# Kernel optimization log

Measured on AMD Instinct MI355X. Metric: run time of the kernel, lower is better.

The kernel has to match this reference:

```python
import jax, jax.numpy as jnp
import numpy as np

B, H, W, C = 8, 128, 128, 64


def setup_inputs() -> dict:
    key = jax.random.key(0)
    x = jax.random.normal(key, (B, H, W, C), dtype=jnp.float32)
    return {"x": x}


def reference(x):
    # Criss-cross affinity: for each pixel (i,j), dot products against
    # the rest of its row (order: k<j then k>j) followed by its full column.
    b, h, w, c = x.shape
    # Row affinities: [B,H,W,W], A_row[b,i,j,k] = <x[b,i,j], x[b,i,k]>
    a_row = jnp.einsum('bijc,bikc->bijk', x, x)
    # Column affinities: [B,H,W,H], A_col[b,i,j,m] = <x[b,i,j], x[b,m,j]>
    a_col = jnp.einsum('bijc,bmjc->bijm', x, x)
    # Remove the self entry k=j from row affinities, preserving order
    # [0..j-1, j+1..W-1] to match the original tf.concat.
    idx = np.array([[k for k in range(w) if k != j] for j in range(w)],
                   dtype=np.int32)  # [W, W-1]
    row_part = jnp.take_along_axis(a_row, jnp.asarray(idx)[None, None, :, :],
                                   axis=3)  # [B,H,W,W-1]
    # Output: [B, H, W, (W-1)+H]
    return jnp.concatenate([row_part, a_col], axis=-1)
```

## Files before the change

kernel.cpp:

```cpp
#include <hip/hip_runtime.h>
#include <hip/hip_bf16.h>
#include <stdint.h>

#define BB 8
#define HH 128
#define WW 128
#define CC 64
#define OUTW 255

#define LDS_STRIDE 72

typedef __attribute__((ext_vector_type(8))) short bf16x8;
typedef __attribute__((ext_vector_type(4))) float f32x4;

__device__ __forceinline__ unsigned short f2bf(float f) {
    union { float f; uint32_t u; } v; v.f = f;
    uint32_t u = v.u;
    return (unsigned short)((u + 0x7FFFu + ((u >> 16) & 1u)) >> 16);
}

__global__ __launch_bounds__(256)
void criss_cross_gram_kernel(const float* __restrict__ x, float* __restrict__ out) {
    __shared__ unsigned short lds[128 * LDS_STRIDE];

    const int g = blockIdx.x;
    const bool isCol = (g >= BB * HH);
    const int gg = isCol ? (g - BB * HH) : g;
    const int b = gg >> 7;
    const int p = gg & 127;

    const float* xbase;
    int xRowStride;
    int outBase;
    int outRowStride;
    if (!isCol) {
        xbase        = x + ((b * HH + p) * WW) * CC;
        xRowStride   = CC;
        outBase      = ((b * HH + p) * WW) * OUTW;
        outRowStride = OUTW;
    } else {
        xbase        = x + (b * HH * WW + p) * CC;
        xRowStride   = WW * CC;
        outBase      = (b * HH * WW + p) * OUTW;
        outRowStride = WW * OUTW;
    }

    const int t = threadIdx.x;

    #pragma unroll
    for (int r = 0; r < 8; ++r) {
        const int idx = r * 256 + t;
        const int row = idx >> 4;
        const int c4  = (idx & 15) << 2;
        const float4 v = *(const float4*)(xbase + row * xRowStride + c4);
        ushort4* dst = (ushort4*)&lds[row * LDS_STRIDE + c4];
        *dst = make_ushort4(f2bf(v.x), f2bf(v.y), f2bf(v.z), f2bf(v.w));
    }
    __syncthreads();

    const int wave = t >> 6;
    const int lane = t & 63;
    const int m16  = lane & 15;
    const int quad = lane >> 4;

    f32x4 acc[2][8];
    #pragma unroll
    for (int rt = 0; rt < 2; ++rt)
        #pragma unroll
        for (int ct = 0; ct < 8; ++ct)
            acc[rt][ct] = (f32x4){0.f, 0.f, 0.f, 0.f};

    #pragma unroll
    for (int ks = 0; ks < 2; ++ks) {
        const int kOff = ks * 32 + quad * 8;
        bf16x8 afrag[2];
        #pragma unroll
        for (int rt = 0; rt < 2; ++rt) {
            const int row = wave * 32 + rt * 16 + m16;
            afrag[rt] = *(const bf16x8*)&lds[row * LDS_STRIDE + kOff];
        }
        #pragma unroll
        for (int ct = 0; ct < 8; ++ct) {
            const int row = ct * 16 + m16;
            const bf16x8 bfrag = *(const bf16x8*)&lds[row * LDS_STRIDE + kOff];
            acc[0][ct] = __builtin_amdgcn_mfma_f32_16x16x32_bf16(afrag[0], bfrag, acc[0][ct], 0, 0, 0);
            acc[1][ct] = __builtin_amdgcn_mfma_f32_16x16x32_bf16(afrag[1], bfrag, acc[1][ct], 0, 0, 0);
        }
    }

    #pragma unroll
    for (int rt = 0; rt < 2; ++rt) {
        #pragma unroll
        for (int reg = 0; reg < 4; ++reg) {
            const int gm = wave * 32 + rt * 16 + quad * 4 + reg;
            float* rowp = out + outBase + gm * outRowStride;
            #pragma unroll
            for (int ct = 0; ct < 8; ++ct) {
                const int gn = ct * 16 + m16;
                const float vv = acc[rt][ct][reg];
                if (!isCol) {
                    if (gn != gm) {
                        rowp[gn - (gn > gm ? 1 : 0)] = vv;
                    }
                } else {
                    rowp[127 + gn] = vv;
                }
            }
        }
    }
}

extern "C" void kernel_launch(void* const* d_in, const int* in_sizes, int n_in,
                              void* d_out, int out_size, void* d_ws, size_t ws_size,
                              hipStream_t stream) {
    const float* x = (const float*)d_in[0];
    float* out = (float*)d_out;
    criss_cross_gram_kernel<<<dim3(BB * HH + BB * WW), dim3(256), 0, stream>>>(x, out);
}
```

Before: 171.1 us.

## Split into column-gram workspace pass and row-gram merge pass with contiguous stores

Computes column affinities into a workspace in a first kernel, then a second kernel computes row affinities and merges them with the workspace column data through LDS, so each output row is written as contiguous vectorized nontemporal stores. The aim is to replace scattered, strided per-element output writes with fully coalesced writes. The cost is an extra round trip of the column Gram through global memory, a second launch, and more LDS per block.

```diff
diff --git a/kernel.cpp b/kernel.cpp
--- a/kernel.cpp
+++ b/kernel.cpp
@@ -1,5 +1,4 @@
 #include <hip/hip_runtime.h>
-#include <hip/hip_bf16.h>
 #include <stdint.h>
 
 #define BB 8
@@ -9,6 +8,7 @@
 #define OUTW 255
 
 #define LDS_STRIDE 72
+#define EPW 255
 
 typedef __attribute__((ext_vector_type(8))) short bf16x8;
 typedef __attribute__((ext_vector_type(4))) float f32x4;
@@ -20,31 +20,14 @@
 }
 
 __global__ __launch_bounds__(256)
-void criss_cross_gram_kernel(const float* __restrict__ x, float* __restrict__ out) {
-    __shared__ unsigned short lds[128 * LDS_STRIDE];
+void cc_pass1_colgram(const float* __restrict__ x, float* __restrict__ ws) {
+    __shared__ unsigned short xs[128 * LDS_STRIDE];
 
     const int g = blockIdx.x;
-    const bool isCol = (g >= BB * HH);
-    const int gg = isCol ? (g - BB * HH) : g;
-    const int b = gg >> 7;
-    const int p = gg & 127;
-
-    const float* xbase;
-    int xRowStride;
-    int outBase;
-    int outRowStride;
-    if (!isCol) {
-        xbase        = x + ((b * HH + p) * WW) * CC;
-        xRowStride   = CC;
-        outBase      = ((b * HH + p) * WW) * OUTW;
-        outRowStride = OUTW;
-    } else {
-        xbase        = x + (b * HH * WW + p) * CC;
-        xRowStride   = WW * CC;
-        outBase      = (b * HH * WW + p) * OUTW;
-        outRowStride = WW * OUTW;
-    }
-
+    const int b = g >> 7;
+    const int j = g & 127;
+    const float* xbase = x + (size_t)(b * HH * WW + j) * CC;
+    float* wbase = ws + (size_t)g * (128 * 128);
     const int t = threadIdx.x;
 
     #pragma unroll
@@ -52,8 +35,8 @@
         const int idx = r * 256 + t;
         const int row = idx >> 4;
         const int c4  = (idx & 15) << 2;
-        const float4 v = *(const float4*)(xbase + row * xRowStride + c4);
-        ushort4* dst = (ushort4*)&lds[row * LDS_STRIDE + c4];
+        const float4 v = *(const float4*)(xbase + (size_t)row * (WW * CC) + c4);
+        ushort4* dst = (ushort4*)&xs[row * LDS_STRIDE + c4];
         *dst = make_ushort4(f2bf(v.x), f2bf(v.y), f2bf(v.z), f2bf(v.w));
     }
     __syncthreads();
@@ -75,14 +58,11 @@
         const int kOff = ks * 32 + quad * 8;
         bf16x8 afrag[2];
         #pragma unroll
-        for (int rt = 0; rt < 2; ++rt) {
-            const int row = wave * 32 + rt * 16 + m16;
-            afrag[rt] = *(const bf16x8*)&lds[row * LDS_STRIDE + kOff];
-        }
+        for (int rt = 0; rt < 2; ++rt)
+            afrag[rt] = *(const bf16x8*)&xs[(wave * 32 + rt * 16 + m16) * LDS_STRIDE + kOff];
         #pragma unroll
         for (int ct = 0; ct < 8; ++ct) {
-            const int row = ct * 16 + m16;
-            const bf16x8 bfrag = *(const bf16x8*)&lds[row * LDS_STRIDE + kOff];
+            const bf16x8 bfrag = *(const bf16x8*)&xs[(ct * 16 + m16) * LDS_STRIDE + kOff];
             acc[0][ct] = __builtin_amdgcn_mfma_f32_16x16x32_bf16(afrag[0], bfrag, acc[0][ct], 0, 0, 0);
             acc[1][ct] = __builtin_amdgcn_mfma_f32_16x16x32_bf16(afrag[1], bfrag, acc[1][ct], 0, 0, 0);
         }
@@ -93,20 +73,108 @@
         #pragma unroll
         for (int reg = 0; reg < 4; ++reg) {
             const int gm = wave * 32 + rt * 16 + quad * 4 + reg;
-            float* rowp = out + outBase + gm * outRowStride;
+            float* rp = wbase + gm * 128;
             #pragma unroll
             for (int ct = 0; ct < 8; ++ct) {
                 const int gn = ct * 16 + m16;
-                const float vv = acc[rt][ct][reg];
-                if (!isCol) {
-                    if (gn != gm) {
-                        rowp[gn - (gn > gm ? 1 : 0)] = vv;
-                    }
-                } else {
-                    rowp[127 + gn] = vv;
+                __builtin_nontemporal_store(acc[rt][ct][reg], &rp[gn]);
+            }
+        }
+    }
+}
+
+__global__ __launch_bounds__(256)
+void cc_pass2_rowgram_merge(const float* __restrict__ x, const float* __restrict__ ws,
+                            float* __restrict__ out) {
+    __shared__ unsigned short xs[128 * LDS_STRIDE];
+    __shared__ float ep[32 * EPW];
+
+    const int g = blockIdx.x;
+    const int b = g >> 7;
+    const int i = g & 127;
+    const float* xbase = x + (size_t)(b * HH + i) * WW * CC;
+    float* obase = out + (size_t)g * (WW * OUTW);
+    const float* wsb = ws + (size_t)b * (128 * 128 * 128);
+    const int t = threadIdx.x;
+
+    #pragma unroll
+    for (int r = 0; r < 8; ++r) {
+        const int idx = r * 256 + t;
+        const int row = idx >> 4;
+        const int c4  = (idx & 15) << 2;
+        const float4 v = *(const float4*)(xbase + row * CC + c4);
+        ushort4* dst = (ushort4*)&xs[row * LDS_STRIDE + c4];
+        *dst = make_ushort4(f2bf(v.x), f2bf(v.y), f2bf(v.z), f2bf(v.w));
+    }
+    __syncthreads();
+
+    const int wave = t >> 6;
+    const int lane = t & 63;
+    const int m16  = lane & 15;
+    const int quad = lane >> 4;
+
+    f32x4 acc[2][8];
+    #pragma unroll
+    for (int c = 0; c < 2; ++c)
+        #pragma unroll
+        for (int r = 0; r < 8; ++r)
+            acc[c][r] = (f32x4){0.f, 0.f, 0.f, 0.f};
+
+    #pragma unroll
+    for (int ks = 0; ks < 2; ++ks) {
+        const int kOff = ks * 32 + quad * 8;
+        bf16x8 bfrag[2];
+        #pragma unroll
+        for (int c = 0; c < 2; ++c)
+            bfrag[c] = *(const bf16x8*)&xs[(wave * 32 + c * 16 + m16) * LDS_STRIDE + kOff];
+        #pragma unroll
+        for (int r = 0; r < 8; ++r) {
+            const bf16x8 afrag = *(const bf16x8*)&xs[(r * 16 + m16) * LDS_STRIDE + kOff];
+            acc[0][r] = __builtin_amdgcn_mfma_f32_16x16x32_bf16(afrag, bfrag[0], acc[0][r], 0, 0, 0);
+            acc[1][r] = __builtin_amdgcn_mfma_f32_16x16x32_bf16(afrag, bfrag[1], acc[1][r], 0, 0, 0);
+        }
+    }
+
+    for (int q = 0; q < 4; ++q) {
+        #pragma unroll
+        for (int rr = 0; rr < 2; ++rr) {
+            const int r = 2 * q + rr;
+            #pragma unroll
+            for (int c = 0; c < 2; ++c) {
+                const int n = wave * 32 + c * 16 + m16;
+                #pragma unroll
+                for (int reg = 0; reg < 4; ++reg) {
+                    const int jl = rr * 16 + quad * 4 + reg;
+                    const int ja = 32 * q + jl;
+                    if (n != ja)
+                        ep[jl * EPW + (n - (n > ja ? 1 : 0))] = acc[c][r][reg];
                 }
             }
         }
+        {
+            const int jl = t >> 3;
+            const int ch = t & 7;
+            const int ja = 32 * q + jl;
+            const float4* src = (const float4*)(wsb + ((size_t)ja * 128 + i) * 128 + ch * 16);
+            float* dst = &ep[jl * EPW + 127 + ch * 16];
+            const float4 v0 = src[0], v1 = src[1], v2 = src[2], v3 = src[3];
+            dst[0]=v0.x; dst[1]=v0.y; dst[2]=v0.z;  dst[3]=v0.w;
+            dst[4]=v1.x; dst[5]=v1.y; dst[6]=v1.z;  dst[7]=v1.w;
+            dst[8]=v2.x; dst[9]=v2.y; dst[10]=v2.z; dst[11]=v2.w;
+            dst[12]=v3.x; dst[13]=v3.y; dst[14]=v3.z; dst[15]=v3.w;
+        }
+        __syncthreads();
+        {
+            const f32x4* eps = (const f32x4*)ep;
+            f32x4* oq = (f32x4*)(obase + q * 32 * OUTW);
+            #pragma unroll
+            for (int s = 0; s < 8; ++s) {
+                const int idx = t + 256 * s;
+                if (idx < 2040)
+                    __builtin_nontemporal_store(eps[idx], &oq[idx]);
+            }
+        }
+        __syncthreads();
     }
 }
 
@@ -115,5 +183,7 @@
                               hipStream_t stream) {
     const float* x = (const float*)d_in[0];
     float* out = (float*)d_out;
-    criss_cross_gram_kernel<<<dim3(BB * HH + BB * WW), dim3(256), 0, stream>>>(x, out);
+    float* ws = (float*)d_ws;
+    cc_pass1_colgram<<<dim3(BB * WW), dim3(256), 0, stream>>>(x, ws);
+    cc_pass2_rowgram_merge<<<dim3(BB * HH), dim3(256), 0, stream>>>(x, ws, out);
 }
```

Result: slower. 205.4 us (+20.0%).
